# Optimization experiments

Measured on AMD Instinct MI355X. Metric: run time of the kernel, lower is better.

The kernel has to match this reference:

```python
import jax, jax.numpy as jnp
import numpy as np

EPS = 1e-5       # BatchNorm2d eps
NHEAD = 8
FILL = -1e30     # stands in for scores_fill_value=-inf (finite for grad safety)


def _proj(x, w, b, g, beta, mean, var):
    # Conv2d 1x1 over NCHW (H=1) == channel matmul, followed by eval-mode BatchNorm2d.
    y = jnp.einsum('oc,bcht->boht', w, x) + b[None, :, None, None]
    inv = g * jax.lax.rsqrt(var + EPS)
    return y * inv[None, :, None, None] + (beta - mean * inv)[None, :, None, None]


def setup_inputs() -> dict:
    rng = jax.random.key(0)
    ks = jax.random.split(rng, 10)
    B, C, T = 8, 512, 1024
    query = jax.random.normal(ks[0], (B, C, 1, T), jnp.float32)
    key = jax.random.normal(ks[1], (B, C, 1, T), jnp.float32)
    value = jax.random.normal(ks[2], (B, C, 1, T), jnp.float32)
    mask = jax.random.randint(ks[3], (B, 1, T, T), 0, 2).astype(jnp.int32)
    Ws = jax.random.normal(ks[4], (4, C, C), jnp.float32) * (1.0 / np.sqrt(C))
    bs = jax.random.normal(ks[5], (4, C), jnp.float32) * 0.1
    gammas = jax.random.uniform(ks[6], (4, C), jnp.float32, 0.5, 1.5)
    betas = jax.random.normal(ks[7], (4, C), jnp.float32) * 0.1
    means = jax.random.normal(ks[8], (4, C), jnp.float32) * 0.1
    vars_ = jax.random.uniform(ks[9], (4, C), jnp.float32, 0.5, 1.5)
    return dict(query=query, key=key, value=value, mask=mask, Ws=Ws, bs=bs,
                gammas=gammas, betas=betas, means=means, vars_=vars_)


def reference(query, key, value, mask, Ws, bs, gammas, betas, means, vars_):
    B, C, _, T1 = query.shape
    T2 = key.shape[3]
    h = NHEAD
    d_k = C // h
    denom = 1.0 / np.sqrt(d_k)

    q = _proj(query, Ws[0], bs[0], gammas[0], betas[0], means[0], vars_[0]).reshape(B, h, d_k, T1)
    k = _proj(key,   Ws[1], bs[1], gammas[1], betas[1], means[1], vars_[1]).reshape(B, h, d_k, T2)
    v = _proj(value, Ws[2], bs[2], gammas[2], betas[2], means[2], vars_[2]).reshape(B, h, d_k, T2)

    # scores = k^T @ q -> (B, h, T2, T1); softmax over key axis (dim=2, matching torch)
    scores = jnp.einsum('bhds,bhdt->bhst', k, q) * denom
    mask0 = jnp.transpose(mask, (0, 1, 3, 2)) == 0  # (B, 1, T2, T1)
    scores = jnp.where(mask0, FILL, scores)
    attn = jax.nn.softmax(scores, axis=2)
    attn = jnp.where(mask0, 0.0, attn)

    # x = v @ attn -> (B, h, d_k, T1) -> (B, C, 1, T1)
    x = jnp.einsum('bhds,bhst->bhdt', v, attn).reshape(B, C, 1, T1)
    out = _proj(x, Ws[3], bs[3], gammas[3], betas[3], means[3], vars_[3])

    # cache=None branch: new_cache = cat(raw key, raw value) along channel dim
    new_cache = jnp.concatenate([key, value], axis=1)
    return (out, new_cache)
```

## Files before the change

### kernel.cpp

```cpp
#include <hip/hip_runtime.h>

typedef unsigned short u16;
typedef unsigned int   u32;
typedef short  bfrag   __attribute__((ext_vector_type(8)));
typedef float  accfrag __attribute__((ext_vector_type(16)));
typedef unsigned int   u32x4 __attribute__((ext_vector_type(4)));
typedef unsigned short u16x4 __attribute__((ext_vector_type(4)));
typedef float          f32x4 __attribute__((ext_vector_type(4)));

#define B_SZ 8
#define C_SZ 512
#define T_SZ 1024
#define NH   8
#define DK   64

#define QSCL 0.18033688f

__device__ __forceinline__ u16 f2bf(float f) {
  u32 u = __float_as_uint(f);
  u = u + 0x7fffu + ((u >> 16) & 1u);
  return (u16)(u >> 16);
}

__device__ __forceinline__ float fexp2(float x) {
  return __builtin_amdgcn_exp2f(x);
}

__device__ __forceinline__ u32 cvtpk(float lo, float hi) {
  u32 r;
  asm("v_cvt_pk_bf16_f32 %0, %1, %2" : "=v"(r) : "v"(lo), "v"(hi));
  return r;
}

__device__ __forceinline__ void permswap(u32 &a, u32 &b) {
  asm volatile("v_permlane32_swap_b32 %0, %1" : "+v"(a), "+v"(b));
}

__device__ __forceinline__ void gload16(const u16* g, u16* l) {
  __builtin_amdgcn_global_load_lds(
      (const __attribute__((address_space(1))) void*)g,
      (__attribute__((address_space(3))) void*)l, 16, 0, 0);
}

__global__ void prep_w(const float* __restrict__ Ws, const float* __restrict__ gam,
                       const float* __restrict__ var, u16* __restrict__ Wp) {
  int idx = blockIdx.x * 256 + threadIdx.x;
  int io = idx >> 9;
  float inv = gam[io] * rsqrtf(var[io] + 1e-5f);
  Wp[idx] = f2bf(Ws[idx] * inv);
}

__global__ void prep_b(const float* __restrict__ bs, const float* __restrict__ gam,
                       const float* __restrict__ beta, const float* __restrict__ mean,
                       const float* __restrict__ var, float* __restrict__ bp) {
  int idx = blockIdx.x * 256 + threadIdx.x;
  float inv = gam[idx] * rsqrtf(var[idx] + 1e-5f);
  bp[idx] = bs[idx] * inv + beta[idx] - mean[idx] * inv;
}

__global__ void transpose_cvt(const float* __restrict__ q, const float* __restrict__ k,
                              const float* __restrict__ v, u16* __restrict__ Xt,
                              float* __restrict__ cache) {
  __shared__ float tile[32][33];
  int z = blockIdx.z;
  int src = z >> 3, b = z & 7;
  const float* in = (src == 0) ? q : ((src == 1) ? k : v);
  u16* out = Xt + (size_t)src * ((size_t)B_SZ * T_SZ * C_SZ);
  int t0 = blockIdx.x * 32, c0 = blockIdx.y * 32;
  int tx = threadIdx.x & 31, ty = threadIdx.x >> 5;
#pragma unroll
  for (int rr = 0; rr < 4; ++rr) {
    int c = c0 + ty + rr * 8;
    float val = in[(((size_t)b * C_SZ + c) << 10) + t0 + tx];
    tile[ty + rr * 8][tx] = val;
    if (src >= 1) {
      int cc = c + (src == 2 ? 512 : 0);
      cache[((size_t)b << 20) + ((size_t)cc << 10) + t0 + tx] = val;
    }
  }
  __syncthreads();
#pragma unroll
  for (int rr = 0; rr < 4; ++rr) {
    int t = t0 + ty + rr * 8;
    out[(((size_t)b << 10) + t) * C_SZ + c0 + tx] = f2bf(tile[tx][ty + rr * 8]);
  }
}

__global__ void mask_bits(const int* __restrict__ mask, u32* __restrict__ mbT) {
  int w = blockIdx.x * 256 + threadIdx.x;
  int bt = w >> 5;
  int st = w & 31;
  const int* mrow = mask + ((size_t)bt << 10) + (st << 5);
  u32 word = 0;
#pragma unroll
  for (int j = 0; j < 32; j += 4) {
    int4 m4 = *(const int4*)(mrow + j);
    word |= (m4.x != 0 ? 1u : 0u) << j;
    word |= (m4.y != 0 ? 1u : 0u) << (j + 1);
    word |= (m4.z != 0 ? 1u : 0u) << (j + 2);
    word |= (m4.w != 0 ? 1u : 0u) << (j + 3);
  }
  int b = bt >> 10, t = bt & 1023;
  mbT[(((size_t)b * 32 + st) << 10) + t] = word;
}

__launch_bounds__(256, 2)
__global__ void gemm_qkv(const u16* __restrict__ Wp, const float* __restrict__ bpA,
                         const u16* __restrict__ Xt,
                         u16* __restrict__ Qf, u16* __restrict__ Kf, u16* __restrict__ Vf) {
  __shared__ __align__(16) u16 lds[2 * 128 * 64];
  int tid = threadIdx.x;
  int src = blockIdx.z >> 3;
  int b   = blockIdx.z & 7;
  int t0 = blockIdx.x * 128;
  int o0 = blockIdx.y * 128;
  int wid = tid >> 6, lane = tid & 63;
  int ln = lane & 31, hi = lane >> 5;
  int wr = wid >> 1, wc = wid & 1;

  const u16* Wsrc = Wp + (size_t)src * 262144;
  const float* bp = bpA + src * 512;
  const u16* Xin  = Xt + (size_t)src * ((size_t)B_SZ * T_SZ * C_SZ);
  u16* Yout = (src == 0) ? Qf : (src == 1 ? Kf : Vf);

  const char* Ag = (const char*)Wsrc;
  const char* Bg = (const char*)(Xin + (((size_t)b << 10) + t0) * C_SZ);
  char* ldsA = (char*)lds;
  char* ldsB = (char*)lds + 16384;

  accfrag acc[2][2];
#pragma unroll
  for (int m2 = 0; m2 < 2; ++m2)
#pragma unroll
    for (int n2 = 0; n2 < 2; ++n2)
#pragma unroll
      for (int e = 0; e < 16; ++e) acc[m2][n2][e] = 0.f;

  int lin = tid * 16;
  u32x4 ra[4], rb[4];
#pragma unroll
  for (int it = 0; it < 4; ++it) {
    int off = lin + it * 4096;
    int r = off >> 7, cb = off & 127;
    ra[it] = *(const u32x4*)(Ag + (size_t)(o0 + r) * 1024 + cb);
    rb[it] = *(const u32x4*)(Bg + (size_t)r * 1024 + cb);
  }

  for (int kt = 0; kt < 8; ++kt) {
    __syncthreads();
#pragma unroll
    for (int it = 0; it < 4; ++it) {
      int off = lin + it * 4096;
      int swz = off ^ (((off >> 7) & 7) << 4);
      *(u32x4*)(ldsA + swz) = ra[it];
      *(u32x4*)(ldsB + swz) = rb[it];
    }
    __syncthreads();
    if (kt < 7) {
#pragma unroll
      for (int it = 0; it < 4; ++it) {
        int off = lin + it * 4096;
        int r = off >> 7, cb = off & 127;
        ra[it] = *(const u32x4*)(Ag + (size_t)(o0 + r) * 1024 + (kt + 1) * 128 + cb);
        rb[it] = *(const u32x4*)(Bg + (size_t)r * 1024 + (kt + 1) * 128 + cb);
      }
    }
#pragma unroll
    for (int kk = 0; kk < 4; ++kk) {
      int csw = (kk * 32 + hi * 16) ^ ((ln & 7) << 4);
      bfrag a[2], bb[2];
#pragma unroll
      for (int m2 = 0; m2 < 2; ++m2)
        a[m2] = *(const bfrag*)(ldsA + (wr * 64 + m2 * 32 + ln) * 128 + csw);
#pragma unroll
      for (int n2 = 0; n2 < 2; ++n2)
        bb[n2] = *(const bfrag*)(ldsB + (wc * 64 + n2 * 32 + ln) * 128 + csw);
#pragma unroll
      for (int m2 = 0; m2 < 2; ++m2)
#pragma unroll
        for (int n2 = 0; n2 < 2; ++n2)
          acc[m2][n2] = __builtin_amdgcn_mfma_f32_32x32x16_bf16(a[m2], bb[n2], acc[m2][n2], 0, 0, 0);
    }
  }

  float oscl = (src == 0) ? QSCL : 1.0f;
#pragma unroll
  for (int m2 = 0; m2 < 2; ++m2) {
    int obase = o0 + wr * 64 + m2 * 32;
#pragma unroll
    for (int n2 = 0; n2 < 2; ++n2) {
      int t = t0 + wc * 64 + n2 * 32 + ln;
      if (src < 2) {
        int tt5 = t & 31, st = t >> 5;
#pragma unroll
        for (int g = 0; g < 4; ++g) {
          int d0 = obase + 8 * g + 4 * hi;
          int hh = d0 >> 6, dd = d0 & 63;
          u16x4 pk4;
#pragma unroll
          for (int qq = 0; qq < 4; ++qq)
            pk4[qq] = f2bf((acc[m2][n2][4 * g + qq] + bp[d0 + qq]) * oscl);
          size_t a = ((((size_t)b * 8 + hh) * 32 + st) << 11)
                   + (size_t)((dd >> 4) * 512 + (tt5 + 32 * ((dd >> 3) & 1)) * 8 + (dd & 7));
          *(u16x4*)(Yout + a) = pk4;
        }
      } else {
        int s = t, st = s >> 5;
#pragma unroll
        for (int r = 0; r < 16; ++r) {
          int d = obase + (r & 3) + 8 * (r >> 2) + 4 * hi;
          int hh = d >> 6, dd = d & 63;
          int fi = ((s >> 4) & 1) * 2 + ((dd >> 5) & 1);
          int l  = (dd & 31) + ((s >> 3) & 1) * 32;
          Yout[((((size_t)b * 8 + hh) * 32 + st) << 11)
               + (size_t)(fi * 512 + l * 8 + (s & 7))] = f2bf(acc[m2][n2][r] + bp[d]);
        }
      }
    }
  }
}

__launch_bounds__(256, 2)
__global__ void gemm_out(const u16* __restrict__ Wp, const float* __restrict__ bp,
                         const u16* __restrict__ Xin, float* __restrict__ Yout) {
  __shared__ __align__(16) u16 lds[2 * 128 * 64];
  int tid = threadIdx.x;
  int b  = blockIdx.z;
  int t0 = blockIdx.x * 128;
  int o0 = blockIdx.y * 128;
  int wid = tid >> 6, lane = tid & 63;
  int ln = lane & 31, hi = lane >> 5;
  int wr = wid >> 1, wc = wid & 1;

  const char* Ag = (const char*)Wp;
  const char* Bg = (const char*)(Xin + (((size_t)b << 10) + t0) * C_SZ);
  char* ldsA = (char*)lds;
  char* ldsB = (char*)lds + 16384;

  accfrag acc[2][2];
#pragma unroll
  for (int m2 = 0; m2 < 2; ++m2)
#pragma unroll
    for (int n2 = 0; n2 < 2; ++n2)
#pragma unroll
      for (int e = 0; e < 16; ++e) acc[m2][n2][e] = 0.f;

  int lin = tid * 16;
  u32x4 ra[4], rb[4];
#pragma unroll
  for (int it = 0; it < 4; ++it) {
    int off = lin + it * 4096;
    int r = off >> 7, cb = off & 127;
    ra[it] = *(const u32x4*)(Ag + (size_t)(o0 + r) * 1024 + cb);
    rb[it] = *(const u32x4*)(Bg + (size_t)r * 1024 + cb);
  }

  for (int kt = 0; kt < 8; ++kt) {
    __syncthreads();
#pragma unroll
    for (int it = 0; it < 4; ++it) {
      int off = lin + it * 4096;
      int swz = off ^ (((off >> 7) & 7) << 4);
      *(u32x4*)(ldsA + swz) = ra[it];
      *(u32x4*)(ldsB + swz) = rb[it];
    }
    __syncthreads();
    if (kt < 7) {
#pragma unroll
      for (int it = 0; it < 4; ++it) {
        int off = lin + it * 4096;
        int r = off >> 7, cb = off & 127;
        ra[it] = *(const u32x4*)(Ag + (size_t)(o0 + r) * 1024 + (kt + 1) * 128 + cb);
        rb[it] = *(const u32x4*)(Bg + (size_t)r * 1024 + (kt + 1) * 128 + cb);
      }
    }
#pragma unroll
    for (int kk = 0; kk < 4; ++kk) {
      int csw = (kk * 32 + hi * 16) ^ ((ln & 7) << 4);
      bfrag a[2], bb[2];
#pragma unroll
      for (int m2 = 0; m2 < 2; ++m2)
        a[m2] = *(const bfrag*)(ldsA + (wr * 64 + m2 * 32 + ln) * 128 + csw);
#pragma unroll
      for (int n2 = 0; n2 < 2; ++n2)
        bb[n2] = *(const bfrag*)(ldsB + (wc * 64 + n2 * 32 + ln) * 128 + csw);
#pragma unroll
      for (int m2 = 0; m2 < 2; ++m2)
#pragma unroll
        for (int n2 = 0; n2 < 2; ++n2)
          acc[m2][n2] = __builtin_amdgcn_mfma_f32_32x32x16_bf16(a[m2], bb[n2], acc[m2][n2], 0, 0, 0);
    }
  }

#pragma unroll
  for (int m2 = 0; m2 < 2; ++m2) {
    int obase = o0 + wr * 64 + m2 * 32;
#pragma unroll
    for (int n2 = 0; n2 < 2; ++n2) {
      int t = t0 + wc * 64 + n2 * 32 + ln;
#pragma unroll
      for (int r = 0; r < 16; ++r) {
        int o = obase + (r & 3) + 8 * (r >> 2) + 4 * hi;
        Yout[(((size_t)b * C_SZ + o) << 10) + t] = acc[m2][n2][r] + bp[o];
      }
    }
  }
}

__launch_bounds__(512, 4)
__global__ void attn_fused(const u16* __restrict__ Qf, const u16* __restrict__ Kf,
                           const u16* __restrict__ Vf, const u32* __restrict__ mbT,
                           u16* __restrict__ X2) {
  __shared__ __align__(16) char smem[33 * 1024];
  u16*   sK   = (u16*)smem;
  u16*   sV   = (u16*)(smem + 16384);
  float* comb = (float*)smem;
  float* mlb  = (float*)(smem + 32768);

  int n = blockIdx.x;
  int bh = n & 63, tb = n >> 6;
  int b = bh >> 3, h = bh & 7;
  int tid = threadIdx.x;
  int wid = tid >> 6, lane = tid & 63;
  int grp = wid >> 2, wl = wid & 3;
  int ln = lane & 31, hi = lane >> 5;
  int tt = tb * 4 + wl;
  int t  = tt * 32 + ln;

  const u16* QfT = Qf + (((size_t)bh * 32 + tt) << 11);
  bfrag qf[4];
#pragma unroll
  for (int j = 0; j < 4; ++j)
    qf[j] = *(const bfrag*)(QfT + j * 512 + lane * 8);

  const u16* KfB = Kf + ((size_t)bh << 16);
  const u16* VfB = Vf + ((size_t)bh << 16);
  const u32* mcol = mbT + ((size_t)b << 15) + t;

  float m_run = -1.0e4f, l_run = 0.f;
  accfrag accd[2];
#pragma unroll
  for (int m2 = 0; m2 < 2; ++m2)
#pragma unroll
    for (int e = 0; e < 16; ++e) accd[m2][e] = 0.f;

  int gtid = tid & 255;
  int soff = gtid * 8;
  u16* sKg = sK + grp * 4096;
  u16* sVg = sV + grp * 4096;
  int st0 = grp * 16;

  gload16(KfB + ((size_t)st0 << 11) + soff, sKg + soff);
  gload16(VfB + ((size_t)st0 << 11) + soff, sVg + soff);
  u32 mw = mcol[st0 << 10];
  __syncthreads();

#pragma unroll 2
  for (int it = 0; it < 16; ++it) {
    int cur = it & 1, nxt = cur ^ 1;
    int st = st0 + it;
    u32 mn = 0;
    if (it < 15) {
      size_t tn = (size_t)(st + 1) << 11;
      gload16(KfB + tn + soff, sKg + nxt * 2048 + soff);
      gload16(VfB + tn + soff, sVg + nxt * 2048 + soff);
      mn = mcol[(st + 1) << 10];
    }

    bfrag kf[4], vf[4];
#pragma unroll
    for (int j = 0; j < 4; ++j) {
      kf[j] = *(const bfrag*)(sKg + cur * 2048 + j * 512 + lane * 8);
      vf[j] = *(const bfrag*)(sVg + cur * 2048 + j * 512 + lane * 8);
    }

    accfrag S;
#pragma unroll
    for (int e = 0; e < 16; ++e) S[e] = 0.f;
#pragma unroll
    for (int j = 0; j < 4; ++j)
      S = __builtin_amdgcn_mfma_f32_32x32x16_bf16(kf[j], qf[j], S, 0, 0, 0);

    u32 mbits = mw >> (4 * hi);
    float p[16];
#pragma unroll
    for (int r = 0; r < 16; ++r) {
      int pos = (r & 3) + 8 * (r >> 2);
      p[r] = ((mbits >> pos) & 1u) ? S[r] : -1e30f;
    }
    float q8[8], q4[4];
#pragma unroll
    for (int r = 0; r < 8; ++r) q8[r] = fmaxf(p[r], p[r + 8]);
#pragma unroll
    for (int r = 0; r < 4; ++r) q4[r] = fmaxf(q8[r], q8[r + 4]);
    float pmax = fmaxf(fmaxf(q4[0], q4[1]), fmaxf(q4[2], q4[3]));
    pmax = fmaxf(pmax, __shfl_xor(pmax, 32));

    if (__any(pmax > m_run + 11.5f)) {
      float m_new = fmaxf(m_run, pmax);
      float alpha = fexp2(m_run - m_new);
      l_run *= alpha;
#pragma unroll
      for (int m2 = 0; m2 < 2; ++m2)
#pragma unroll
        for (int e = 0; e < 16; ++e) accd[m2][e] *= alpha;
      m_run = m_new;
    }

#pragma unroll
    for (int r = 0; r < 16; ++r)
      p[r] = fexp2(p[r] - m_run);
    float s8[8], s4[4];
#pragma unroll
    for (int r = 0; r < 8; ++r) s8[r] = p[r] + p[r + 8];
#pragma unroll
    for (int r = 0; r < 4; ++r) s4[r] = s8[r] + s8[r + 4];
    float psum = (s4[0] + s4[1]) + (s4[2] + s4[3]);
    psum += __shfl_xor(psum, 32);
    l_run += psum;

    bfrag pf[2];
#pragma unroll
    for (int j2 = 0; j2 < 2; ++j2) {
      u32 A0 = cvtpk(p[8 * j2 + 0], p[8 * j2 + 1]);
      u32 A1 = cvtpk(p[8 * j2 + 2], p[8 * j2 + 3]);
      u32 B0 = cvtpk(p[8 * j2 + 4], p[8 * j2 + 5]);
      u32 B1 = cvtpk(p[8 * j2 + 6], p[8 * j2 + 7]);
      permswap(A0, B0);
      permswap(A1, B1);
      union { u32 u[4]; bfrag f; } pu;
      pu.u[0] = A0; pu.u[1] = A1; pu.u[2] = B0; pu.u[3] = B1;
      pf[j2] = pu.f;
    }
#pragma unroll
    for (int j2 = 0; j2 < 2; ++j2)
#pragma unroll
      for (int m2 = 0; m2 < 2; ++m2)
        accd[m2] = __builtin_amdgcn_mfma_f32_32x32x16_bf16(vf[j2 * 2 + m2], pf[j2], accd[m2], 0, 0, 0);

    __syncthreads();
    mw = mn;
  }

  if (grp == 1) {
#pragma unroll
    for (int m2 = 0; m2 < 2; ++m2)
#pragma unroll
      for (int e = 0; e < 16; ++e)
        comb[wl * 2048 + (m2 * 16 + e) * 64 + lane] = accd[m2][e];
    if (hi == 0) {
      mlb[(wl * 32 + ln) * 2]     = m_run;
      mlb[(wl * 32 + ln) * 2 + 1] = l_run;
    }
  }
  __syncthreads();
  if (grp == 0) {
    float m1v = mlb[(wl * 32 + ln) * 2];
    float l1v = mlb[(wl * 32 + ln) * 2 + 1];
    float M  = fmaxf(m_run, m1v);
    float w0 = fexp2(m_run - M), w1 = fexp2(m1v - M);
    float l  = l_run * w0 + l1v * w1;
    float invl = (l > 0.f) ? 1.f / l : 0.f;
    u16* Orow = X2 + (((size_t)b << 10) + t) * C_SZ + h * DK;
#pragma unroll
    for (int m2 = 0; m2 < 2; ++m2)
#pragma unroll
      for (int g = 0; g < 4; ++g) {
        u16x4 pk4;
#pragma unroll
        for (int qq = 0; qq < 4; ++qq) {
          int e = 4 * g + qq;
          float v2 = comb[wl * 2048 + (m2 * 16 + e) * 64 + lane];
          pk4[qq] = f2bf((accd[m2][e] * w0 + v2 * w1) * invl);
        }
        *(u16x4*)(Orow + m2 * 32 + 8 * g + 4 * hi) = pk4;
      }
  }
}

extern "C" void kernel_launch(void* const* d_in, const int* in_sizes, int n_in,
                              void* d_out, int out_size, void* d_ws, size_t ws_size,
                              hipStream_t stream) {
  (void)in_sizes; (void)n_in; (void)out_size; (void)ws_size;
  const float* q    = (const float*)d_in[0];
  const float* k    = (const float*)d_in[1];
  const float* v    = (const float*)d_in[2];
  const int*   mask = (const int*)d_in[3];
  const float* Ws   = (const float*)d_in[4];
  const float* bs   = (const float*)d_in[5];
  const float* gam  = (const float*)d_in[6];
  const float* beta = (const float*)d_in[7];
  const float* mean = (const float*)d_in[8];
  const float* var  = (const float*)d_in[9];

  float* out   = (float*)d_out;
  float* cache = out + (size_t)B_SZ * C_SZ * T_SZ;

  const size_t ARR = (size_t)B_SZ * T_SZ * C_SZ;
  char* ws = (char*)d_ws;
  u16*   Wp = (u16*)(ws);
  float* bp = (float*)(ws + 2097152);
  u16*   Xt = (u16*)(ws + 2162688);
  u16*   Qt = Xt + 3 * ARR;
  u16*   Kt = Qt + ARR;
  u16*   Vb = Kt + ARR;
  u16*   X2 = Vb + ARR;
  u32*   mb = (u32*)((char*)(X2 + ARR));

  prep_w<<<4096, 256, 0, stream>>>(Ws, gam, var, Wp);
  prep_b<<<8, 256, 0, stream>>>(bs, gam, beta, mean, var, bp);
  transpose_cvt<<<dim3(32, 16, 24), 256, 0, stream>>>(q, k, v, Xt, cache);
  mask_bits<<<1024, 256, 0, stream>>>(mask, mb);

  gemm_qkv<<<dim3(8, 4, 24), 256, 0, stream>>>(Wp, bp, Xt, Qt, Kt, Vb);
  attn_fused<<<512, 512, 0, stream>>>(Qt, Kt, Vb, mb, X2);
  gemm_out<<<dim3(8, 4, 8), 256, 0, stream>>>(Wp + 786432, bp + 1536, X2, out);
}
```

Baseline: 97.63 us.

## Merge weight/bias prep, shrink gemm_out tile, raise occupancy, prioritize MFMA

Result: faster. 95.59 us (-2.1%).

```diff
diff --git a/kernel.cpp b/kernel.cpp
--- a/kernel.cpp
+++ b/kernel.cpp
@@ -42,20 +42,21 @@
       (__attribute__((address_space(3))) void*)l, 16, 0, 0);
 }
 
-__global__ void prep_w(const float* __restrict__ Ws, const float* __restrict__ gam,
-                       const float* __restrict__ var, u16* __restrict__ Wp) {
-  int idx = blockIdx.x * 256 + threadIdx.x;
-  int io = idx >> 9;
-  float inv = gam[io] * rsqrtf(var[io] + 1e-5f);
-  Wp[idx] = f2bf(Ws[idx] * inv);
-}
-
-__global__ void prep_b(const float* __restrict__ bs, const float* __restrict__ gam,
-                       const float* __restrict__ beta, const float* __restrict__ mean,
-                       const float* __restrict__ var, float* __restrict__ bp) {
-  int idx = blockIdx.x * 256 + threadIdx.x;
-  float inv = gam[idx] * rsqrtf(var[idx] + 1e-5f);
-  bp[idx] = bs[idx] * inv + beta[idx] - mean[idx] * inv;
+__global__ void prep_wb(const float* __restrict__ Ws, const float* __restrict__ bs,
+                        const float* __restrict__ gam, const float* __restrict__ beta,
+                        const float* __restrict__ mean, const float* __restrict__ var,
+                        u16* __restrict__ Wp, float* __restrict__ bp) {
+  int bx = blockIdx.x;
+  if (bx < 4096) {
+    int idx = bx * 256 + threadIdx.x;
+    int io = idx >> 9;
+    float inv = gam[io] * rsqrtf(var[io] + 1e-5f);
+    Wp[idx] = f2bf(Ws[idx] * inv);
+  } else {
+    int idx = (bx - 4096) * 256 + threadIdx.x;
+    float inv = gam[idx] * rsqrtf(var[idx] + 1e-5f);
+    bp[idx] = bs[idx] * inv + beta[idx] - mean[idx] * inv;
+  }
 }
 
 __global__ void transpose_cvt(const float* __restrict__ q, const float* __restrict__ k,
@@ -104,7 +105,7 @@
   mbT[(((size_t)b * 32 + st) << 10) + t] = word;
 }
 
-__launch_bounds__(256, 2)
+__launch_bounds__(256, 4)
 __global__ void gemm_qkv(const u16* __restrict__ Wp, const float* __restrict__ bpA,
                          const u16* __restrict__ Xt,
                          u16* __restrict__ Qf, u16* __restrict__ Kf, u16* __restrict__ Vf) {
@@ -220,13 +221,13 @@
   }
 }
 
-__launch_bounds__(256, 2)
+__launch_bounds__(256, 4)
 __global__ void gemm_out(const u16* __restrict__ Wp, const float* __restrict__ bp,
                          const u16* __restrict__ Xin, float* __restrict__ Yout) {
-  __shared__ __align__(16) u16 lds[2 * 128 * 64];
+  __shared__ __align__(16) char ldsc[24576];
   int tid = threadIdx.x;
   int b  = blockIdx.z;
-  int t0 = blockIdx.x * 128;
+  int t0 = blockIdx.x * 64;
   int o0 = blockIdx.y * 128;
   int wid = tid >> 6, lane = tid & 63;
   int ln = lane & 31, hi = lane >> 5;
@@ -234,24 +235,27 @@
 
   const char* Ag = (const char*)Wp;
   const char* Bg = (const char*)(Xin + (((size_t)b << 10) + t0) * C_SZ);
-  char* ldsA = (char*)lds;
-  char* ldsB = (char*)lds + 16384;
-
-  accfrag acc[2][2];
+  char* ldsA = ldsc;
+  char* ldsB = ldsc + 16384;
+
+  accfrag acc[2];
 #pragma unroll
   for (int m2 = 0; m2 < 2; ++m2)
 #pragma unroll
-    for (int n2 = 0; n2 < 2; ++n2)
-#pragma unroll
-      for (int e = 0; e < 16; ++e) acc[m2][n2][e] = 0.f;
+    for (int e = 0; e < 16; ++e) acc[m2][e] = 0.f;
 
   int lin = tid * 16;
-  u32x4 ra[4], rb[4];
+  u32x4 ra[4], rb[2];
 #pragma unroll
   for (int it = 0; it < 4; ++it) {
     int off = lin + it * 4096;
     int r = off >> 7, cb = off & 127;
     ra[it] = *(const u32x4*)(Ag + (size_t)(o0 + r) * 1024 + cb);
+  }
+#pragma unroll
+  for (int it = 0; it < 2; ++it) {
+    int off = lin + it * 4096;
+    int r = off >> 7, cb = off & 127;
     rb[it] = *(const u32x4*)(Bg + (size_t)r * 1024 + cb);
   }
 
@@ -262,6 +266,11 @@
       int off = lin + it * 4096;
       int swz = off ^ (((off >> 7) & 7) << 4);
       *(u32x4*)(ldsA + swz) = ra[it];
+    }
+#pragma unroll
+    for (int it = 0; it < 2; ++it) {
+      int off = lin + it * 4096;
+      int swz = off ^ (((off >> 7) & 7) << 4);
       *(u32x4*)(ldsB + swz) = rb[it];
     }
     __syncthreads();
@@ -271,38 +280,36 @@
         int off = lin + it * 4096;
         int r = off >> 7, cb = off & 127;
         ra[it] = *(const u32x4*)(Ag + (size_t)(o0 + r) * 1024 + (kt + 1) * 128 + cb);
+      }
+#pragma unroll
+      for (int it = 0; it < 2; ++it) {
+        int off = lin + it * 4096;
+        int r = off >> 7, cb = off & 127;
         rb[it] = *(const u32x4*)(Bg + (size_t)r * 1024 + (kt + 1) * 128 + cb);
       }
     }
 #pragma unroll
     for (int kk = 0; kk < 4; ++kk) {
       int csw = (kk * 32 + hi * 16) ^ ((ln & 7) << 4);
-      bfrag a[2], bb[2];
+      bfrag a[2], bb;
 #pragma unroll
       for (int m2 = 0; m2 < 2; ++m2)
         a[m2] = *(const bfrag*)(ldsA + (wr * 64 + m2 * 32 + ln) * 128 + csw);
-#pragma unroll
-      for (int n2 = 0; n2 < 2; ++n2)
-        bb[n2] = *(const bfrag*)(ldsB + (wc * 64 + n2 * 32 + ln) * 128 + csw);
+      bb = *(const bfrag*)(ldsB + (wc * 32 + ln) * 128 + csw);
 #pragma unroll
       for (int m2 = 0; m2 < 2; ++m2)
-#pragma unroll
-        for (int n2 = 0; n2 < 2; ++n2)
-          acc[m2][n2] = __builtin_amdgcn_mfma_f32_32x32x16_bf16(a[m2], bb[n2], acc[m2][n2], 0, 0, 0);
+        acc[m2] = __builtin_amdgcn_mfma_f32_32x32x16_bf16(a[m2], bb, acc[m2], 0, 0, 0);
     }
   }
 
 #pragma unroll
   for (int m2 = 0; m2 < 2; ++m2) {
     int obase = o0 + wr * 64 + m2 * 32;
-#pragma unroll
-    for (int n2 = 0; n2 < 2; ++n2) {
-      int t = t0 + wc * 64 + n2 * 32 + ln;
-#pragma unroll
-      for (int r = 0; r < 16; ++r) {
-        int o = obase + (r & 3) + 8 * (r >> 2) + 4 * hi;
-        Yout[(((size_t)b * C_SZ + o) << 10) + t] = acc[m2][n2][r] + bp[o];
-      }
+    int t = t0 + wc * 32 + ln;
+#pragma unroll
+    for (int r = 0; r < 16; ++r) {
+      int o = obase + (r & 3) + 8 * (r >> 2) + 4 * hi;
+      Yout[(((size_t)b * C_SZ + o) << 10) + t] = acc[m2][r] + bp[o];
     }
   }
 }
@@ -377,9 +384,11 @@
     accfrag S;
 #pragma unroll
     for (int e = 0; e < 16; ++e) S[e] = 0.f;
+    __builtin_amdgcn_s_setprio(1);
 #pragma unroll
     for (int j = 0; j < 4; ++j)
       S = __builtin_amdgcn_mfma_f32_32x32x16_bf16(kf[j], qf[j], S, 0, 0, 0);
+    __builtin_amdgcn_s_setprio(0);
 
     u32 mbits = mw >> (4 * hi);
     float p[16];
@@ -432,11 +441,13 @@
       pu.u[0] = A0; pu.u[1] = A1; pu.u[2] = B0; pu.u[3] = B1;
       pf[j2] = pu.f;
     }
+    __builtin_amdgcn_s_setprio(1);
 #pragma unroll
     for (int j2 = 0; j2 < 2; ++j2)
 #pragma unroll
       for (int m2 = 0; m2 < 2; ++m2)
         accd[m2] = __builtin_amdgcn_mfma_f32_32x32x16_bf16(vf[j2 * 2 + m2], pf[j2], accd[m2], 0, 0, 0);
+    __builtin_amdgcn_s_setprio(0);
 
     __syncthreads();
     mw = mn;
@@ -507,12 +518,11 @@
   u16*   X2 = Vb + ARR;
   u32*   mb = (u32*)((char*)(X2 + ARR));
 
-  prep_w<<<4096, 256, 0, stream>>>(Ws, gam, var, Wp);
-  prep_b<<<8, 256, 0, stream>>>(bs, gam, beta, mean, var, bp);
+  prep_wb<<<4104, 256, 0, stream>>>(Ws, bs, gam, beta, mean, var, Wp, bp);
   transpose_cvt<<<dim3(32, 16, 24), 256, 0, stream>>>(q, k, v, Xt, cache);
   mask_bits<<<1024, 256, 0, stream>>>(mask, mb);
 
   gemm_qkv<<<dim3(8, 4, 24), 256, 0, stream>>>(Wp, bp, Xt, Qt, Kt, Vb);
   attn_fused<<<512, 512, 0, stream>>>(Qt, Kt, Vb, mb, X2);
-  gemm_out<<<dim3(8, 4, 8), 256, 0, stream>>>(Wp + 786432, bp + 1536, X2, out);
-}
+  gemm_out<<<dim3(16, 4, 8), 256, 0, stream>>>(Wp + 786432, bp + 1536, X2, out);
+}
```
